# Performance work log

Measured on AMD Instinct MI355X. Metric: run time of the kernel, lower is better.

## Reference

```python
import jax, jax.numpy as jnp
import numpy as np

B, N, E, IN_DIM, OUT_DIM = 8, 4500, 72000, 128, 128
EPS = 1e-5  # torch LayerNorm default


def setup_inputs() -> dict:
    key = jax.random.key(0)
    k0, k1, k2 = jax.random.split(key, 3)
    node_features = jax.random.normal(k0, (B, N, IN_DIM), dtype=jnp.float32)
    edge_index = jax.random.randint(k1, (B, 2, E), 0, N, dtype=jnp.int64)
    node_mask = jnp.ones((B, N), dtype=jnp.float32)
    edge_mask = jnp.ones((B, E), dtype=jnp.float32)
    W = (jax.random.normal(k2, (OUT_DIM, IN_DIM), dtype=jnp.float32)
         / np.float32(np.sqrt(IN_DIM)))
    b = jnp.zeros((OUT_DIM,), dtype=jnp.float32)
    gamma = jnp.ones((OUT_DIM,), dtype=jnp.float32)
    beta = jnp.zeros((OUT_DIM,), dtype=jnp.float32)
    return {"node_features": node_features, "edge_index": edge_index,
            "node_mask": node_mask, "edge_mask": edge_mask,
            "W": W, "b": b, "gamma": gamma, "beta": beta}


def reference(node_features, edge_index, node_mask, edge_mask, W, b, gamma, beta):
    Bsz, Nn, _ = node_features.shape
    # linear transform: h = x W^T + b  -> [B, N, out_dim]
    h = jnp.einsum('bni,oi->bno', node_features, W) + b
    D = h.shape[-1]
    total = Bsz * Nn

    # With all nodes valid, the sparse index of node (b, n) is b*Nn + n.
    offsets = (jnp.arange(Bsz, dtype=edge_index.dtype) * Nn)[:, None]  # [B,1]
    src = (edge_index[:, 0, :] + offsets).reshape(-1)  # [B*E]
    tgt = (edge_index[:, 1, :] + offsets).reshape(-1)  # [B*E]
    ew = edge_mask.reshape(-1)                          # [B*E] edge validity

    flat_h = h.reshape(total, D)

    # in-degree (valid edges only) + self-loop, D^{-1/2} normalization
    deg = jax.ops.segment_sum(ew, tgt, num_segments=total) + 1.0
    dinv = deg ** -0.5

    coef = dinv[src] * dinv[tgt] * ew                   # [B*E]
    msg = flat_h[src] * coef[:, None]                   # gather + weight
    agg = jax.ops.segment_sum(msg, tgt, num_segments=total)
    agg = agg + flat_h * dinv[:, None]                  # self contribution

    h = h + agg.reshape(Bsz, Nn, D)                     # residual

    # dropout is identity at inference; LayerNorm then ReLU then mask
    mu = jnp.mean(h, axis=-1, keepdims=True)
    var = jnp.mean((h - mu) ** 2, axis=-1, keepdims=True)
    h = (h - mu) / jnp.sqrt(var + EPS) * gamma + beta
    h = jax.nn.relu(h) * node_mask[..., None]
    return h
```

## Files before the change

kernel.cpp:

```cpp
#include <hip/hip_runtime.h>
#include <math.h>

typedef unsigned short ushort_t;
typedef unsigned int uint_t;
typedef __attribute__((ext_vector_type(8))) short bf16x8;
typedef __attribute__((ext_vector_type(16))) float f32x16;

constexpr int Bc   = 8;
constexpr int Nn   = 4500;
constexpr int Ec   = 72000;
constexpr int D    = 128;
constexpr int T    = Bc * Nn;
constexpr int TE   = Bc * Ec;
constexpr float EPS = 1e-5f;

constexpr int PAD = 32;
constexpr int RST = 64;

constexpr int NB_W    = 64;
constexpr int NB_Z    = (T * PAD / 4) / 256;
constexpr int NB_PREP = NB_W + NB_Z;

constexpr int NB_ECH  = (Ec + 255) / 256;
constexpr int NB_EDGE = 8 * NB_ECH;

constexpr int NB_GEMM = ((T / 32) * 2 + 3) / 4;
constexpr int NB_DINV = 8 * 18;
constexpr int NB_GD   = NB_GEMM + NB_DINV;

constexpr size_t WS_CNTP  = 0;
constexpr size_t WS_EDATA = 4608000;
constexpr size_t WS_DINV  = 13824000;
constexpr size_t WS_WHI   = 13968000;
constexpr size_t WS_WLO   = 14000768;
constexpr size_t WS_H     = 14033536;

__device__ __forceinline__ ushort_t f32_to_bf16_rne(float f) {
  uint_t u = __float_as_uint(f);
  uint_t r = (u + 0x7fffu + ((u >> 16) & 1u)) >> 16;
  return (ushort_t)r;
}
__device__ __forceinline__ float bf16_to_f32(ushort_t h) {
  return __uint_as_float(((uint_t)h) << 16);
}

__global__ __launch_bounds__(256) void prep_kernel(
    const float* __restrict__ W, ushort_t* __restrict__ Whi,
    ushort_t* __restrict__ Wlo, int4* __restrict__ cntp4) {
  const int bid = blockIdx.x;
  if (bid < NB_W) {
    int i = bid * 256 + threadIdx.x;
    float w = W[i];
    ushort_t hi = f32_to_bf16_rne(w);
    Whi[i] = hi;
    Wlo[i] = f32_to_bf16_rne(w - bf16_to_f32(hi));
  } else {
    int i = (bid - NB_W) * 256 + threadIdx.x;
    cntp4[i] = make_int4(0, 0, 0, 0);
  }
}

__global__ __launch_bounds__(256) void edge_kernel(
    const int* __restrict__ ei, const float* __restrict__ em,
    int* __restrict__ cntp, uint_t* __restrict__ edata) {
  const int b  = blockIdx.x & 7;
  const int el = (blockIdx.x >> 3) * 256 + threadIdx.x;
  if (el >= Ec) return;
  const int* eb = ei + b * 2 * Ec;
  int t0 = eb[Ec + el];
  if ((unsigned)t0 >= (unsigned)Nn) return;
  int tg = t0 + b * Nn;
  int rk = atomicAdd(&cntp[(size_t)tg * PAD], 1);
  if (rk >= RST) return;
  int s0 = eb[el];
  float ew = em[b * Ec + el];
  uint_t sl = (uint_t)s0;
  if ((unsigned)s0 >= (unsigned)Nn) { sl = 0; ew = 0.f; }
  uint_t pk = ((uint_t)f32_to_bf16_rne(ew) << 16) | sl;
  edata[(size_t)tg * RST + rk] = pk;
}

__global__ __launch_bounds__(256) void gemm_dinv_kernel(
    const float* __restrict__ x, const ushort_t* __restrict__ Whi,
    const ushort_t* __restrict__ Wlo, const float* __restrict__ bias,
    ushort_t* __restrict__ h, const uint_t* __restrict__ edata,
    const int* __restrict__ cntp, float* __restrict__ dinv) {
  const int bid = blockIdx.x;
  if (bid < NB_GEMM) {
    const int g = bid * 4 + (threadIdx.x >> 6);
    if (g >= (T / 32) * 2) return;
    const int lane = threadIdx.x & 63;
    const int mt = g >> 1;
    const int nh = g & 1;
    const int m0 = mt * 32;
    const int r  = lane & 31;
    const int kh = lane >> 5;

    const float* xrow = x + (size_t)(m0 + r) * D + kh * 8;

    f32x16 acc[2];
#pragma unroll
    for (int n = 0; n < 2; ++n)
#pragma unroll
      for (int j = 0; j < 16; ++j) acc[n][j] = 0.f;

#pragma unroll
    for (int ks = 0; ks < 8; ++ks) {
      const float4 p0 = ((const float4*)(xrow + ks * 16))[0];
      const float4 p1 = ((const float4*)(xrow + ks * 16))[1];
      const float xa[8] = {p0.x, p0.y, p0.z, p0.w, p1.x, p1.y, p1.z, p1.w};
      bf16x8 ahi, alo;
#pragma unroll
      for (int j = 0; j < 8; ++j) {
        ushort_t hb = f32_to_bf16_rne(xa[j]);
        ahi[j] = (short)hb;
        alo[j] = (short)f32_to_bf16_rne(xa[j] - bf16_to_f32(hb));
      }
#pragma unroll
      for (int n = 0; n < 2; ++n) {
        const size_t boff = (size_t)((nh * 2 + n) * 32 + r) * D + ks * 16 + kh * 8;
        bf16x8 bhi = *(const bf16x8*)(Whi + boff);
        bf16x8 blo = *(const bf16x8*)(Wlo + boff);
        acc[n] = __builtin_amdgcn_mfma_f32_32x32x16_bf16(ahi, bhi, acc[n], 0, 0, 0);
        acc[n] = __builtin_amdgcn_mfma_f32_32x32x16_bf16(ahi, blo, acc[n], 0, 0, 0);
        acc[n] = __builtin_amdgcn_mfma_f32_32x32x16_bf16(alo, bhi, acc[n], 0, 0, 0);
      }
    }

#pragma unroll
    for (int n = 0; n < 2; ++n) {
      const int col = (nh * 2 + n) * 32 + r;
      const float bv = bias[col];
#pragma unroll
      for (int j = 0; j < 16; ++j) {
        const int mrow = m0 + (j & 3) + 8 * (j >> 2) + 4 * kh;
        h[(size_t)mrow * D + col] = f32_to_bf16_rne(acc[n][j] + bv);
      }
    }
  } else {
    const int zb = bid - NB_GEMM;
    const int b  = zb & 7;
    const int nl = (zb >> 3) * 256 + threadIdx.x;
    if (nl >= Nn) return;
    const int i = b * Nn + nl;
    int cnt = cntp[(size_t)i * PAD];
    cnt = (cnt > RST) ? RST : cnt;
    const uint_t* row = edata + (size_t)i * RST;
    float s = 0.f;
    for (int j = 0; j < cnt; ++j) s += bf16_to_f32((ushort_t)(row[j] >> 16));
    dinv[i] = 1.0f / sqrtf(s + 1.0f);
  }
}

__global__ __launch_bounds__(256) void gather_ln_kernel(
    const ushort_t* __restrict__ h, const int* __restrict__ cntp,
    const uint_t* __restrict__ edata, const float* __restrict__ dinv,
    const float* __restrict__ gamma, const float* __restrict__ beta,
    const float* __restrict__ mask, float* __restrict__ out) {
  const int bid  = blockIdx.x;
  const int b    = bid & 7;
  const int wid  = threadIdx.x >> 6;
  const int node = b * Nn + (bid >> 3) * 4 + wid;
  const int bOff = b * Nn;
  const int lane = threadIdx.x & 63;
  const int f4   = lane & 31;
  const int half = lane >> 5;

  const ushort4* h4 = (const ushort4*)h;
  int cnt = cntp[(size_t)node * PAD];
  cnt = (cnt > RST) ? RST : cnt;
  const uint_t* row = edata + (size_t)node * RST;

  ushort4 hq = h4[(size_t)node * 32 + f4];
  float4 hv = make_float4(bf16_to_f32(hq.x), bf16_to_f32(hq.y),
                          bf16_to_f32(hq.z), bf16_to_f32(hq.w));

  float4 accE = make_float4(0.f, 0.f, 0.f, 0.f);
  int i = half;
  for (; i + 6 < cnt; i += 8) {
    uint_t p0 = row[i];
    uint_t p1 = row[i + 2];
    uint_t p2 = row[i + 4];
    uint_t p3 = row[i + 6];
    int sg0 = bOff + (p0 & 0xFFFFu);
    int sg1 = bOff + (p1 & 0xFFFFu);
    int sg2 = bOff + (p2 & 0xFFFFu);
    int sg3 = bOff + (p3 & 0xFFFFu);
    float c0 = dinv[sg0] * bf16_to_f32((ushort_t)(p0 >> 16));
    float c1 = dinv[sg1] * bf16_to_f32((ushort_t)(p1 >> 16));
    float c2 = dinv[sg2] * bf16_to_f32((ushort_t)(p2 >> 16));
    float c3 = dinv[sg3] * bf16_to_f32((ushort_t)(p3 >> 16));
    ushort4 q0 = h4[(size_t)sg0 * 32 + f4];
    ushort4 q1 = h4[(size_t)sg1 * 32 + f4];
    ushort4 q2 = h4[(size_t)sg2 * 32 + f4];
    ushort4 q3 = h4[(size_t)sg3 * 32 + f4];
    accE.x += bf16_to_f32(q0.x) * c0 + bf16_to_f32(q1.x) * c1 +
              bf16_to_f32(q2.x) * c2 + bf16_to_f32(q3.x) * c3;
    accE.y += bf16_to_f32(q0.y) * c0 + bf16_to_f32(q1.y) * c1 +
              bf16_to_f32(q2.y) * c2 + bf16_to_f32(q3.y) * c3;
    accE.z += bf16_to_f32(q0.z) * c0 + bf16_to_f32(q1.z) * c1 +
              bf16_to_f32(q2.z) * c2 + bf16_to_f32(q3.z) * c3;
    accE.w += bf16_to_f32(q0.w) * c0 + bf16_to_f32(q1.w) * c1 +
              bf16_to_f32(q2.w) * c2 + bf16_to_f32(q3.w) * c3;
  }
  for (; i < cnt; i += 2) {
    uint_t p0 = row[i];
    int sg0 = bOff + (p0 & 0xFFFFu);
    float c0 = dinv[sg0] * bf16_to_f32((ushort_t)(p0 >> 16));
    ushort4 q0 = h4[(size_t)sg0 * 32 + f4];
    accE.x += bf16_to_f32(q0.x) * c0;
    accE.y += bf16_to_f32(q0.y) * c0;
    accE.z += bf16_to_f32(q0.z) * c0;
    accE.w += bf16_to_f32(q0.w) * c0;
  }

  accE.x += __shfl_xor(accE.x, 32);
  accE.y += __shfl_xor(accE.y, 32);
  accE.z += __shfl_xor(accE.z, 32);
  accE.w += __shfl_xor(accE.w, 32);

  const float dt = dinv[node];
  float4 acc;
  acc.x = hv.x * (1.f + dt) + dt * accE.x;
  acc.y = hv.y * (1.f + dt) + dt * accE.y;
  acc.z = hv.z * (1.f + dt) + dt * accE.z;
  acc.w = hv.w * (1.f + dt) + dt * accE.w;

  float su = acc.x + acc.y + acc.z + acc.w;
  float ss = acc.x * acc.x + acc.y * acc.y + acc.z * acc.z + acc.w * acc.w;
#pragma unroll
  for (int o = 16; o > 0; o >>= 1) {
    su += __shfl_xor(su, o);
    ss += __shfl_xor(ss, o);
  }
  float mu  = su * (1.0f / 128.0f);
  float var = ss * (1.0f / 128.0f) - mu * mu;
  float rs  = 1.0f / sqrtf(var + EPS);
  float m   = mask[node];

  float4 g  = ((const float4*)gamma)[f4];
  float4 bb = ((const float4*)beta)[f4];
  float4 rv;
  rv.x = fmaxf((acc.x - mu) * rs * g.x + bb.x, 0.f) * m;
  rv.y = fmaxf((acc.y - mu) * rs * g.y + bb.y, 0.f) * m;
  rv.z = fmaxf((acc.z - mu) * rs * g.z + bb.z, 0.f) * m;
  rv.w = fmaxf((acc.w - mu) * rs * g.w + bb.w, 0.f) * m;
  if (half == 0) ((float4*)out)[(size_t)node * 32 + f4] = rv;
}

extern "C" void kernel_launch(void* const* d_in, const int* in_sizes, int n_in,
                              void* d_out, int out_size, void* d_ws, size_t ws_size,
                              hipStream_t stream) {
  const float* x     = (const float*)d_in[0];
  const int*   ei    = (const int*)d_in[1];
  const float* nmask = (const float*)d_in[2];
  const float* emask = (const float*)d_in[3];
  const float* W     = (const float*)d_in[4];
  const float* bias  = (const float*)d_in[5];
  const float* gamma = (const float*)d_in[6];
  const float* beta  = (const float*)d_in[7];
  float* out = (float*)d_out;

  char*     ws    = (char*)d_ws;
  int*      cntp  = (int*)     (ws + WS_CNTP);
  uint_t*   edata = (uint_t*)  (ws + WS_EDATA);
  float*    dinv  = (float*)   (ws + WS_DINV);
  ushort_t* Whi   = (ushort_t*)(ws + WS_WHI);
  ushort_t* Wlo   = (ushort_t*)(ws + WS_WLO);
  ushort_t* h     = (ushort_t*)(ws + WS_H);

  prep_kernel<<<NB_PREP, 256, 0, stream>>>(W, Whi, Wlo, (int4*)cntp);
  edge_kernel<<<NB_EDGE, 256, 0, stream>>>(ei, emask, cntp, edata);
  gemm_dinv_kernel<<<NB_GD, 256, 0, stream>>>(x, Whi, Wlo, bias, h,
                                              edata, cntp, dinv);
  gather_ln_kernel<<<T / 4, 256, 0, stream>>>(h, cntp, edata, dinv,
                                              gamma, beta, nmask, out);
}
```

Before: 81.22 us.

## Restructure GEMM so each block owns a 32-row tile across all output columns

The GEMM part of the fused gemm/dinv kernel now gives each block one 32-row M tile, with its four waves each computing one 32-column slice. Previously each wave computed two column tiles of a row tile, and two waves shared a row tile across block boundaries. Sharing x rows inside a block improves cache reuse of the activation reads and halves accumulator registers per wave, which may raise occupancy. Tiles are mapped to blocks interleaved by batch index, likely to line up with L2/XCD locality. Each wave now converts the same x row to bf16 hi/lo redundantly, and there are more blocks, some of which exit early.

Measured after the change: 82.45 us. About the same (+1.5%).

```diff
diff --git a/kernel.cpp b/kernel.cpp
--- a/kernel.cpp
+++ b/kernel.cpp
@@ -24,9 +24,9 @@
 constexpr int NB_ECH  = (Ec + 255) / 256;
 constexpr int NB_EDGE = 8 * NB_ECH;
 
-constexpr int NB_GEMM = ((T / 32) * 2 + 3) / 4;
-constexpr int NB_DINV = 8 * 18;
-constexpr int NB_GD   = NB_GEMM + NB_DINV;
+constexpr int NB_GEMMP = 8 * 141;
+constexpr int NB_DINV  = 8 * 18;
+constexpr int NB_GD    = NB_GEMMP + NB_DINV;
 
 constexpr size_t WS_CNTP  = 0;
 constexpr size_t WS_EDATA = 4608000;
@@ -86,23 +86,24 @@
     ushort_t* __restrict__ h, const uint_t* __restrict__ edata,
     const int* __restrict__ cntp, float* __restrict__ dinv) {
   const int bid = blockIdx.x;
-  if (bid < NB_GEMM) {
-    const int g = bid * 4 + (threadIdx.x >> 6);
-    if (g >= (T / 32) * 2) return;
+  if (bid < NB_GEMMP) {
+    const int b = bid & 7;
+    const int q = bid >> 3;
+    const int ct0 = (b * 1125 + 4) >> 3;
+    const int ct1 = ((b + 1) * 1125 + 4) >> 3;
+    if (q >= ct1 - ct0) return;
+    const int mt = ct0 + q;
+    const int m0 = mt * 32;
+    const int ct = threadIdx.x >> 6;
     const int lane = threadIdx.x & 63;
-    const int mt = g >> 1;
-    const int nh = g & 1;
-    const int m0 = mt * 32;
     const int r  = lane & 31;
     const int kh = lane >> 5;
 
     const float* xrow = x + (size_t)(m0 + r) * D + kh * 8;
 
-    f32x16 acc[2];
-#pragma unroll
-    for (int n = 0; n < 2; ++n)
-#pragma unroll
-      for (int j = 0; j < 16; ++j) acc[n][j] = 0.f;
+    f32x16 acc;
+#pragma unroll
+    for (int j = 0; j < 16; ++j) acc[j] = 0.f;
 
 #pragma unroll
     for (int ks = 0; ks < 8; ++ks) {
@@ -116,29 +117,23 @@
         ahi[j] = (short)hb;
         alo[j] = (short)f32_to_bf16_rne(xa[j] - bf16_to_f32(hb));
       }
-#pragma unroll
-      for (int n = 0; n < 2; ++n) {
-        const size_t boff = (size_t)((nh * 2 + n) * 32 + r) * D + ks * 16 + kh * 8;
-        bf16x8 bhi = *(const bf16x8*)(Whi + boff);
-        bf16x8 blo = *(const bf16x8*)(Wlo + boff);
-        acc[n] = __builtin_amdgcn_mfma_f32_32x32x16_bf16(ahi, bhi, acc[n], 0, 0, 0);
-        acc[n] = __builtin_amdgcn_mfma_f32_32x32x16_bf16(ahi, blo, acc[n], 0, 0, 0);
-        acc[n] = __builtin_amdgcn_mfma_f32_32x32x16_bf16(alo, bhi, acc[n], 0, 0, 0);
-      }
+      const size_t boff = (size_t)(ct * 32 + r) * D + ks * 16 + kh * 8;
+      bf16x8 bhi = *(const bf16x8*)(Whi + boff);
+      bf16x8 blo = *(const bf16x8*)(Wlo + boff);
+      acc = __builtin_amdgcn_mfma_f32_32x32x16_bf16(ahi, bhi, acc, 0, 0, 0);
+      acc = __builtin_amdgcn_mfma_f32_32x32x16_bf16(ahi, blo, acc, 0, 0, 0);
+      acc = __builtin_amdgcn_mfma_f32_32x32x16_bf16(alo, bhi, acc, 0, 0, 0);
     }
 
-#pragma unroll
-    for (int n = 0; n < 2; ++n) {
-      const int col = (nh * 2 + n) * 32 + r;
-      const float bv = bias[col];
-#pragma unroll
-      for (int j = 0; j < 16; ++j) {
-        const int mrow = m0 + (j & 3) + 8 * (j >> 2) + 4 * kh;
-        h[(size_t)mrow * D + col] = f32_to_bf16_rne(acc[n][j] + bv);
-      }
+    const int col = ct * 32 + r;
+    const float bv = bias[col];
+#pragma unroll
+    for (int j = 0; j < 16; ++j) {
+      const int mrow = m0 + (j & 3) + 8 * (j >> 2) + 4 * kh;
+      h[(size_t)mrow * D + col] = f32_to_bf16_rne(acc[j] + bv);
     }
   } else {
-    const int zb = bid - NB_GEMM;
+    const int zb = bid - NB_GEMMP;
     const int b  = zb & 7;
     const int nl = (zb >> 3) * 256 + threadIdx.x;
     if (nl >= Nn) return;
```
